# Kernel tuning notes

Hardware: AMD Instinct MI355X
Metric: run time of the kernel (lower is better)

The kernel has to match this reference:

```python
import jax, jax.numpy as jnp
import numpy as np

L, H, HS, D, T, V, B = 6, 6, 64, 384, 256, 65, 64
EPS = 1e-5


def layer_norm(x, g, b):
    m = x.mean(-1, keepdims=True)
    v = x.var(-1, keepdims=True)
    return (x - m) / jnp.sqrt(v + EPS) * g + b


def setup_inputs() -> dict:
    key = jax.random.key(0)
    ks = jax.random.split(key, 12)
    s = 0.02
    return {
        "idx": jax.random.randint(ks[0], (B, T), 0, V),
        "targets": jax.random.randint(ks[1], (B, T), 0, V),
        "tok_emb": s * jax.random.normal(ks[2], (V, D), jnp.float32),
        "pos_emb": s * jax.random.normal(ks[3], (T, D), jnp.float32),
        "Wq": s * jax.random.normal(ks[4], (L, H, D, HS), jnp.float32),
        "Wk": s * jax.random.normal(ks[5], (L, H, D, HS), jnp.float32),
        "Wv": s * jax.random.normal(ks[6], (L, H, D, HS), jnp.float32),
        "Wproj": s * jax.random.normal(ks[7], (L, D, D), jnp.float32),
        "bproj": jnp.zeros((L, D), jnp.float32),
        "W1": s * jax.random.normal(ks[8], (L, D, 4 * D), jnp.float32),
        "b1": jnp.zeros((L, 4 * D), jnp.float32),
        "W2": s * jax.random.normal(ks[9], (L, 4 * D, D), jnp.float32),
        "b2": jnp.zeros((L, D), jnp.float32),
        "ln1_g": jnp.ones((L, D), jnp.float32),
        "ln1_b": jnp.zeros((L, D), jnp.float32),
        "lnf_g": jnp.ones((D,), jnp.float32),
        "lnf_b": jnp.zeros((D,), jnp.float32),
        "Whead": s * jax.random.normal(ks[10], (D, V), jnp.float32),
        "bhead": jnp.zeros((V,), jnp.float32),
    }


def reference(idx, targets, tok_emb, pos_emb, Wq, Wk, Wv, Wproj, bproj,
              W1, b1, W2, b2, ln1_g, ln1_b, lnf_g, lnf_b, Whead, bhead):
    b, t = idx.shape
    x = tok_emb[idx] + pos_emb[:t]  # [B,T,D]
    mask = jnp.tril(jnp.ones((t, t), bool))
    scale = x.shape[-1] ** -0.5  # NOTE: original scales by n_emb_d**-0.5, not head_size**-0.5
    for l in range(L):
        y = layer_norm(x, ln1_g[l], ln1_b[l])
        q = jnp.einsum('btd,hde->bhte', y, Wq[l])
        k = jnp.einsum('btd,hde->bhte', y, Wk[l])
        v = jnp.einsum('btd,hde->bhte', y, Wv[l])
        w = jnp.einsum('bhte,bhse->bhts', q, k) * scale
        w = jnp.where(mask, w, -jnp.inf)
        w = jax.nn.softmax(w, axis=-1)
        o = jnp.einsum('bhts,bhse->bhte', w, v)
        o = o.transpose(0, 2, 1, 3).reshape(b, t, H * HS)  # concat heads on last dim
        x = x + o @ Wproj[l] + bproj[l]
        # NOTE: original Block reuses ln1 (not ln2) before the FFN -- replicated faithfully
        y2 = layer_norm(x, ln1_g[l], ln1_b[l])
        x = x + jax.nn.relu(y2 @ W1[l] + b1[l]) @ W2[l] + b2[l]
    x = layer_norm(x, lnf_g, lnf_b)
    logits = x @ Whead + bhead  # [B,T,V]
    logp = jax.nn.log_softmax(logits, axis=-1)
    loss = -jnp.take_along_axis(logp, targets[..., None], axis=-1).mean()
    return logits, loss
```

## Files before the change

kernel.cpp:

```cpp
#include <hip/hip_runtime.h>
#include <math.h>

#define L_ 6
#define H_ 6
#define HS_ 64
#define D_ 384
#define T_ 256
#define V_ 65
#define B_ 64
#define ROWS (B_*T_)
#define QKVN 1152
#define EPS_ 1e-5f

typedef __attribute__((ext_vector_type(8))) __bf16 bf16x8;
typedef __attribute__((ext_vector_type(4))) float f32x4;

__device__ __forceinline__ bf16x8 u4_to_bf8(uint4 u) {
    return __builtin_bit_cast(bf16x8, u);
}

__device__ __forceinline__ void glds16(const void* g, void* l) {
    __builtin_amdgcn_global_load_lds(
        (const __attribute__((address_space(1))) void*)g,
        (__attribute__((address_space(3))) void*)l, 16, 0, 0);
}

__global__ void embed_kernel(const int* __restrict__ idx,
                             const float* __restrict__ tok,
                             const float* __restrict__ pos,
                             float* __restrict__ x) {
    int i = blockIdx.x * blockDim.x + threadIdx.x;
    int d = i % D_;
    int row = i / D_;
    int t = row % T_;
    x[i] = tok[idx[row]*D_ + d] + pos[t*D_ + d];
}

__global__ __launch_bounds__(256)
void ln4(const float* __restrict__ x,
         const float* __restrict__ g,
         const float* __restrict__ b,
         __bf16* __restrict__ yb) {
    int w = threadIdx.x >> 6, lane = threadIdx.x & 63;
    int row = blockIdx.x * 4 + w;
    const float* xr = x + (size_t)row * D_;
    float v[6];
    #pragma unroll
    for (int i = 0; i < 6; ++i) v[i] = xr[lane + 64*i];
    float s = 0.f, sq = 0.f;
    #pragma unroll
    for (int i = 0; i < 6; ++i) { s += v[i]; sq += v[i]*v[i]; }
    for (int off = 32; off; off >>= 1) {
        s  += __shfl_xor(s,  off);
        sq += __shfl_xor(sq, off);
    }
    float mean = s * (1.0f/D_);
    float var  = sq * (1.0f/D_) - mean*mean;
    float rstd = rsqrtf(var + EPS_);
    __bf16* yr = yb + (size_t)row * D_;
    #pragma unroll
    for (int i = 0; i < 6; ++i) {
        int c = lane + 64*i;
        yr[c] = (__bf16)((v[i]-mean)*rstd*g[c] + b[c]);
    }
}

__global__ __launch_bounds__(256)
void transpose_cast(const float* __restrict__ src, __bf16* __restrict__ dst,
                    int R, int C, int zdiv, long sA, long sB, long dbase)
{
    __shared__ float tile[32][33];
    int z = blockIdx.z;
    const float* s = src + (long)z * R * C;
    __bf16* d = dst + dbase + (long)(z / zdiv) * sA + (long)(z % zdiv) * sB;
    int c0 = blockIdx.x * 32, r0 = blockIdx.y * 32;
    int t = threadIdx.x;
    int tr = t >> 3, tc = (t & 7) * 4;
    float4 v = *(const float4*)(s + (long)(r0 + tr) * C + c0 + tc);
    tile[tr][tc+0] = v.x; tile[tr][tc+1] = v.y;
    tile[tr][tc+2] = v.z; tile[tr][tc+3] = v.w;
    __syncthreads();
    #pragma unroll
    for (int j = 0; j < 4; ++j)
        d[(long)(c0 + tr) * R + r0 + tc + j] = (__bf16)tile[tc+j][tr];
}

__global__ __launch_bounds__(256)
void head_prep(const float* __restrict__ Whead, __bf16* __restrict__ headT) {
    int i = blockIdx.x * 256 + threadIdx.x;
    int n = i / D_, k = i % D_;
    headT[i] = (n < V_) ? (__bf16)Whead[k*V_ + n] : (__bf16)0.0f;
}

template<int TM>
__global__ __launch_bounds__(256)
void gemm_t(const __bf16* __restrict__ A, const __bf16* __restrict__ Bt,
            const float* __restrict__ bias, const float* res,
            float* outF, __bf16* outB,
            int K, int ldc, int ncols, int relu)
{
    constexpr int MI = TM / 32;
    __shared__ __align__(16) __bf16 As[2][TM*32];
    __shared__ __align__(16) __bf16 Bs[2][128*32];
    int t = threadIdx.x;
    int w = t >> 6, lane = t & 63;
    int ln = lane & 15, quad = lane >> 4;
    int n0 = blockIdx.x * 128, m0 = blockIdx.y * TM;
    int wm = (w >> 1) * (TM/2), wn = (w & 1) * 64;

    f32x4 acc[MI][4] = {};

    const char* Ab = (const char*)A + (size_t)m0 * K * 2;
    const char* Bb = (const char*)Bt + (size_t)n0 * K * 2;
    int f0 = w*64 + lane, f1 = f0 + 256;
    int r0 = f0 >> 2, r1 = f1 >> 2;
    size_t ga0 = (size_t)r0 * K * 2 + (size_t)(((f0 & 3) ^ (r0 & 3)) * 16);
    size_t ga1 = (size_t)r1 * K * 2 + (size_t)(((f1 & 3) ^ (r1 & 3)) * 16);
    int lo0 = w*64*16, lo1 = (w*64 + 256)*16;

    int nIt = K >> 5;
    glds16(Ab + ga0, (char*)As[0] + lo0);
    if constexpr (TM == 128) glds16(Ab + ga1, (char*)As[0] + lo1);
    glds16(Bb + ga0, (char*)Bs[0] + lo0);
    glds16(Bb + ga1, (char*)Bs[0] + lo1);

    for (int it = 0; it < nIt; ++it) {
        int p = it & 1;
        __syncthreads();
        if (it + 1 < nIt) {
            size_t kb = (size_t)(it + 1) * 64;
            glds16(Ab + ga0 + kb, (char*)As[p^1] + lo0);
            if constexpr (TM == 128) glds16(Ab + ga1 + kb, (char*)As[p^1] + lo1);
            glds16(Bb + ga0 + kb, (char*)Bs[p^1] + lo0);
            glds16(Bb + ga1 + kb, (char*)Bs[p^1] + lo1);
        }
        bf16x8 af[MI], bfr[4];
        #pragma unroll
        for (int i = 0; i < MI; ++i) {
            int row = wm + i*16 + ln;
            af[i] = __builtin_bit_cast(bf16x8,
                *(const uint4*)&As[p][row*32 + ((quad ^ (row & 3)) * 8)]);
        }
        #pragma unroll
        for (int j = 0; j < 4; ++j) {
            int row = wn + j*16 + ln;
            bfr[j] = __builtin_bit_cast(bf16x8,
                *(const uint4*)&Bs[p][row*32 + ((quad ^ (row & 3)) * 8)]);
        }
        #pragma unroll
        for (int i = 0; i < MI; ++i)
            #pragma unroll
            for (int j = 0; j < 4; ++j)
                acc[i][j] = __builtin_amdgcn_mfma_f32_16x16x32_bf16(
                                af[i], bfr[j], acc[i][j], 0, 0, 0);
        __syncthreads();
    }
    #pragma unroll
    for (int i = 0; i < MI; ++i) {
        #pragma unroll
        for (int r = 0; r < 4; ++r) {
            int row = m0 + wm + i*16 + quad*4 + r;
            #pragma unroll
            for (int j = 0; j < 4; ++j) {
                int col = n0 + wn + j*16 + ln;
                if (col < ncols) {
                    float v = acc[i][j][r];
                    if (bias) v += bias[col];
                    if (relu) v = fmaxf(v, 0.f);
                    if (res)  v += res[(size_t)row*ldc + col];
                    if (outF) outF[(size_t)row*ldc + col] = v;
                    if (outB) outB[(size_t)row*ldc + col] = (__bf16)v;
                }
            }
        }
    }
}

__global__ __launch_bounds__(256, 2)
void attn4(const __bf16* __restrict__ qkv, __bf16* __restrict__ o)
{
    __shared__ __align__(16) __bf16 Ks[256*72];
    __shared__ __align__(16) __bf16 Vt[64*264];
    __shared__ __align__(16) __bf16 Pw[4][32*40];
    int bid = blockIdx.x;
    int h = bid % H_;
    int b = bid / H_;
    int t = threadIdx.x;
    int w = t >> 6, lane = t & 63;
    int ln = lane & 15, quad = lane >> 4;
    const size_t rowb = (size_t)b * T_ * QKVN;
    const int hoff = h * HS_;
    const float scale = 0.05103103630798288f;

    for (int c = t; c < 2048; c += 256) {
        int r = c >> 3, e0 = (c & 7) * 8;
        uint4 uk = *(const uint4*)(qkv + rowb + (size_t)r*QKVN + 384 + hoff + e0);
        *(uint4*)&Ks[r*72 + e0] = uk;
        uint4 uv = *(const uint4*)(qkv + rowb + (size_t)r*QKVN + 768 + hoff + e0);
        bf16x8 v8 = u4_to_bf8(uv);
        #pragma unroll
        for (int j = 0; j < 8; ++j) {
            int e = e0 + j;
            Vt[e*264 + (((r >> 3) ^ ((e >> 3) & 3)) * 8) + (r & 7)] = v8[j];
        }
    }

    int qis[2] = { w, 7 - w };
    uint4 Qf[2][2][2];
    #pragma unroll
    for (int tl = 0; tl < 2; ++tl)
        #pragma unroll
        for (int mi = 0; mi < 2; ++mi)
            #pragma unroll
            for (int kc = 0; kc < 2; ++kc)
                Qf[tl][mi][kc] = *(const uint4*)(qkv + rowb +
                    (size_t)(qis[tl]*32 + mi*16 + ln)*QKVN + hoff + kc*32 + quad*8);

    __syncthreads();

    __bf16* P = Pw[w];
    #pragma unroll
    for (int tl = 0; tl < 2; ++tl) {
        int qi = qis[tl];
        f32x4 O[2][4] = {};
        float mst[2][4], lst[2][4];
        #pragma unroll
        for (int mi = 0; mi < 2; ++mi)
            #pragma unroll
            for (int r = 0; r < 4; ++r) { mst[mi][r] = -INFINITY; lst[mi][r] = 0.f; }

        for (int st = 0; st <= qi; ++st) {
            int sb = st * 32;
            f32x4 S[2][2] = {};
            #pragma unroll
            for (int kc = 0; kc < 2; ++kc) {
                uint4 Kf[2];
                #pragma unroll
                for (int ji = 0; ji < 2; ++ji)
                    Kf[ji] = *(const uint4*)&Ks[(sb + ji*16 + ln)*72 + kc*32 + quad*8];
                #pragma unroll
                for (int mi = 0; mi < 2; ++mi) {
                    bf16x8 qa = __builtin_bit_cast(bf16x8, Qf[tl][mi][kc]);
                    #pragma unroll
                    for (int ji = 0; ji < 2; ++ji)
                        S[mi][ji] = __builtin_amdgcn_mfma_f32_16x16x32_bf16(
                            qa, __builtin_bit_cast(bf16x8, Kf[ji]), S[mi][ji], 0, 0, 0);
                }
            }
            int diag = (st == qi);
            #pragma unroll
            for (int mi = 0; mi < 2; ++mi)
                #pragma unroll
                for (int ji = 0; ji < 2; ++ji)
                    #pragma unroll
                    for (int r = 0; r < 4; ++r) {
                        float v = S[mi][ji][r] * scale;
                        if (diag && (ji*16 + ln) > (mi*16 + quad*4 + r)) v = -INFINITY;
                        S[mi][ji][r] = v;
                    }
            #pragma unroll
            for (int mi = 0; mi < 2; ++mi)
                #pragma unroll
                for (int r = 0; r < 4; ++r) {
                    float mx = fmaxf(S[mi][0][r], S[mi][1][r]);
                    #pragma unroll
                    for (int off = 1; off < 16; off <<= 1)
                        mx = fmaxf(mx, __shfl_xor(mx, off));
                    float mn = fmaxf(mst[mi][r], mx);
                    float al = __expf(mst[mi][r] - mn);
                    mst[mi][r] = mn;
                    float p0 = __expf(S[mi][0][r] - mn);
                    float p1 = __expf(S[mi][1][r] - mn);
                    S[mi][0][r] = p0; S[mi][1][r] = p1;
                    float rs = p0 + p1;
                    #pragma unroll
                    for (int off = 1; off < 16; off <<= 1)
                        rs += __shfl_xor(rs, off);
                    lst[mi][r] = lst[mi][r]*al + rs;
                    #pragma unroll
                    for (int ei = 0; ei < 4; ++ei) O[mi][ei][r] *= al;
                }
            #pragma unroll
            for (int mi = 0; mi < 2; ++mi)
                #pragma unroll
                for (int ji = 0; ji < 2; ++ji)
                    #pragma unroll
                    for (int r = 0; r < 4; ++r)
                        P[(mi*16 + quad*4 + r)*40 + ji*16 + ln] = (__bf16)S[mi][ji][r];
            uint4 Pf[2], Vf[4];
            #pragma unroll
            for (int mi = 0; mi < 2; ++mi)
                Pf[mi] = *(const uint4*)&P[(mi*16 + ln)*40 + quad*8];
            #pragma unroll
            for (int ei = 0; ei < 4; ++ei) {
                int e = ei*16 + ln;
                Vf[ei] = *(const uint4*)&Vt[e*264 + (((st*4 + quad) ^ ((e >> 3) & 3)) * 8)];
            }
            #pragma unroll
            for (int mi = 0; mi < 2; ++mi)
                #pragma unroll
                for (int ei = 0; ei < 4; ++ei)
                    O[mi][ei] = __builtin_amdgcn_mfma_f32_16x16x32_bf16(
                        __builtin_bit_cast(bf16x8, Pf[mi]),
                        __builtin_bit_cast(bf16x8, Vf[ei]), O[mi][ei], 0, 0, 0);
        }
        #pragma unroll
        for (int mi = 0; mi < 2; ++mi)
            #pragma unroll
            for (int r = 0; r < 4; ++r) {
                float inv = 1.0f / lst[mi][r];
                size_t row = (size_t)(b*T_ + qi*32 + mi*16 + quad*4 + r);
                #pragma unroll
                for (int ei = 0; ei < 4; ++ei)
                    o[row*D_ + hoff + ei*16 + ln] = (__bf16)(O[mi][ei][r] * inv);
            }
    }
}

__global__ __launch_bounds__(256)
void loss2(const float* __restrict__ logits,
           const int* __restrict__ tg,
           float* __restrict__ loss)
{
    int row = blockIdx.x * 256 + threadIdx.x;
    const float* lr = logits + (size_t)row * V_;
    float m = -INFINITY;
    for (int c = 0; c < V_; ++c) m = fmaxf(m, lr[c]);
    float s = 0.f;
    for (int c = 0; c < V_; ++c) s += __expf(lr[c] - m);
    float val = -(lr[tg[row]] - m - __logf(s)) * (1.0f/ROWS);
    for (int off = 32; off; off >>= 1) val += __shfl_xor(val, off);
    __shared__ float red[4];
    int w = threadIdx.x >> 6, lane = threadIdx.x & 63;
    if (lane == 0) red[w] = val;
    __syncthreads();
    if (threadIdx.x == 0)
        atomicAdd(loss, red[0]+red[1]+red[2]+red[3]);
}

extern "C" void kernel_launch(void* const* d_in, const int* in_sizes, int n_in,
                              void* d_out, int out_size, void* d_ws, size_t ws_size,
                              hipStream_t stream)
{
    const int*   idx     = (const int*)  d_in[0];
    const int*   targets = (const int*)  d_in[1];
    const float* tok     = (const float*)d_in[2];
    const float* pos     = (const float*)d_in[3];
    const float* Wq      = (const float*)d_in[4];
    const float* Wk      = (const float*)d_in[5];
    const float* Wv      = (const float*)d_in[6];
    const float* Wproj   = (const float*)d_in[7];
    const float* bproj   = (const float*)d_in[8];
    const float* W1      = (const float*)d_in[9];
    const float* b1      = (const float*)d_in[10];
    const float* W2      = (const float*)d_in[11];
    const float* b2      = (const float*)d_in[12];
    const float* ln1g    = (const float*)d_in[13];
    const float* ln1b    = (const float*)d_in[14];
    const float* lnfg    = (const float*)d_in[15];
    const float* lnfb    = (const float*)d_in[16];
    const float* Whead   = (const float*)d_in[17];
    const float* bhead   = (const float*)d_in[18];

    float* logits = (float*)d_out;
    float* loss   = logits + (size_t)ROWS * V_;

    const size_t SZ = (size_t)ROWS * D_;
    const size_t RGELEMS = (size_t)ROWS * 4 * D_;

    float*  x   = (float*)d_ws;
    __bf16* yb  = (__bf16*)(x + SZ);
    __bf16* Rg  = yb + SZ;
    __bf16* qkv = Rg;
    __bf16* hid = Rg;
    __bf16* o   = Rg + RGELEMS;
    __bf16* qkvT  = o + SZ;
    __bf16* projT = qkvT + (size_t)L_*QKVN*D_;
    __bf16* w1T   = projT + (size_t)L_*D_*D_;
    __bf16* w2T   = w1T + (size_t)L_*D_*4*D_;
    __bf16* headT = w2T + (size_t)L_*D_*4*D_;

    transpose_cast<<<dim3(2,12,36),256,0,stream>>>(Wq, qkvT, D_, HS_, H_,
        (long)QKVN*D_, (long)HS_*D_, 0L);
    transpose_cast<<<dim3(2,12,36),256,0,stream>>>(Wk, qkvT, D_, HS_, H_,
        (long)QKVN*D_, (long)HS_*D_, (long)D_*D_);
    transpose_cast<<<dim3(2,12,36),256,0,stream>>>(Wv, qkvT, D_, HS_, H_,
        (long)QKVN*D_, (long)HS_*D_, 2L*D_*D_);
    transpose_cast<<<dim3(12,12,6),256,0,stream>>>(Wproj, projT, D_, D_, 1,
        (long)D_*D_, 0L, 0L);
    transpose_cast<<<dim3(48,12,6),256,0,stream>>>(W1, w1T, D_, 4*D_, 1,
        (long)D_*4*D_, 0L, 0L);
    transpose_cast<<<dim3(12,48,6),256,0,stream>>>(W2, w2T, 4*D_, D_, 1,
        (long)D_*4*D_, 0L, 0L);
    head_prep<<<(128*D_)/256, 256, 0, stream>>>(Whead, headT);

    embed_kernel<<<(ROWS*D_)/256, 256, 0, stream>>>(idx, tok, pos, x);

    for (int l = 0; l < L_; ++l) {
        ln4<<<ROWS/4, 256, 0, stream>>>(x, ln1g + l*D_, ln1b + l*D_, yb);
        gemm_t<128><<<dim3(QKVN/128, ROWS/128), 256, 0, stream>>>(
            yb, qkvT + (size_t)l*QKVN*D_, nullptr, nullptr, nullptr, qkv,
            D_, QKVN, QKVN, 0);
        attn4<<<B_*H_, 256, 0, stream>>>(qkv, o);
        gemm_t<64><<<dim3(D_/128, ROWS/64), 256, 0, stream>>>(
            o, projT + (size_t)l*D_*D_, bproj + l*D_, x, x, nullptr,
            D_, D_, D_, 0);
        ln4<<<ROWS/4, 256, 0, stream>>>(x, ln1g + l*D_, ln1b + l*D_, yb);
        gemm_t<128><<<dim3(4*D_/128, ROWS/128), 256, 0, stream>>>(
            yb, w1T + (size_t)l*D_*4*D_, b1 + l*4*D_, nullptr, nullptr, hid,
            D_, 4*D_, 4*D_, 1);
        gemm_t<64><<<dim3(D_/128, ROWS/64), 256, 0, stream>>>(
            hid, w2T + (size_t)l*D_*4*D_, b2 + l*D_, x, x, nullptr,
            4*D_, D_, D_, 0);
    }
    ln4<<<ROWS/4, 256, 0, stream>>>(x, lnfg, lnfb, yb);
    gemm_t<64><<<dim3(1, ROWS/64), 256, 0, stream>>>(
        yb, headT, bhead, nullptr, logits, nullptr,
        D_, V_, V_, 0);
    hipMemsetAsync(loss, 0, sizeof(float), stream);
    loss2<<<ROWS/256, 256, 0, stream>>>(logits, targets, loss);
}
```

Before: 1.529 ms.

## Add A-stationary GEMM keeping full K=384 row tile in LDS, streaming B from global

```diff
diff --git a/kernel.cpp b/kernel.cpp
--- a/kernel.cpp
+++ b/kernel.cpp
@@ -90,6 +90,80 @@
     int i = blockIdx.x * 256 + threadIdx.x;
     int n = i / D_, k = i % D_;
     headT[i] = (n < V_) ? (__bf16)Whead[k*V_ + n] : (__bf16)0.0f;
+}
+
+__global__ __launch_bounds__(256)
+void gemm_as(const __bf16* __restrict__ A, const __bf16* __restrict__ Bt,
+             const float* __restrict__ bias, const float* res,
+             float* outF, __bf16* outB,
+             int N, int ldc, int ncols, int relu)
+{
+    __shared__ __align__(16) __bf16 As[64*392];
+    int t = threadIdx.x;
+    int w = t >> 6, lane = t & 63;
+    int ln = lane & 15, quad = lane >> 4;
+    int m0 = blockIdx.x * 64;
+
+    for (int c = t; c < 3072; c += 256) {
+        int r = c / 48, ch = c - r*48;
+        uint4 v = *(const uint4*)(A + (size_t)(m0 + r)*384 + ch*8);
+        *(uint4*)&As[r*392 + ch*8] = v;
+    }
+    __syncthreads();
+
+    int nch = N >> 6;
+    for (int nc = w; nc < nch; nc += 4) {
+        int n0 = nc * 64;
+        const __bf16* Bp = Bt + (size_t)n0 * 384;
+        f32x4 acc[4][4] = {};
+        uint4 bcur[4], bnxt[4];
+        #pragma unroll
+        for (int j = 0; j < 4; ++j)
+            bcur[j] = *(const uint4*)(Bp + (size_t)(j*16 + ln)*384 + quad*8);
+        #pragma unroll
+        for (int kc = 0; kc < 12; ++kc) {
+            if (kc < 11) {
+                #pragma unroll
+                for (int j = 0; j < 4; ++j)
+                    bnxt[j] = *(const uint4*)(Bp + (size_t)(j*16 + ln)*384
+                                              + (kc+1)*32 + quad*8);
+            }
+            uint4 af[4];
+            #pragma unroll
+            for (int i = 0; i < 4; ++i)
+                af[i] = *(const uint4*)&As[(i*16 + ln)*392 + kc*32 + quad*8];
+            #pragma unroll
+            for (int i = 0; i < 4; ++i)
+                #pragma unroll
+                for (int j = 0; j < 4; ++j)
+                    acc[i][j] = __builtin_amdgcn_mfma_f32_16x16x32_bf16(
+                        __builtin_bit_cast(bf16x8, af[i]),
+                        __builtin_bit_cast(bf16x8, bcur[j]), acc[i][j], 0, 0, 0);
+            if (kc < 11) {
+                #pragma unroll
+                for (int j = 0; j < 4; ++j) bcur[j] = bnxt[j];
+            }
+        }
+        #pragma unroll
+        for (int i = 0; i < 4; ++i) {
+            #pragma unroll
+            for (int r = 0; r < 4; ++r) {
+                int row = m0 + i*16 + quad*4 + r;
+                #pragma unroll
+                for (int j = 0; j < 4; ++j) {
+                    int col = n0 + j*16 + ln;
+                    if (col < ncols) {
+                        float v = acc[i][j][r];
+                        if (bias) v += bias[col];
+                        if (relu) v = fmaxf(v, 0.f);
+                        if (res)  v += res[(size_t)row*ldc + col];
+                        if (outF) outF[(size_t)row*ldc + col] = v;
+                        if (outB) outB[(size_t)row*ldc + col] = (__bf16)v;
+                    }
+                }
+            }
+        }
+    }
 }
 
 template<int TM>
@@ -398,25 +472,25 @@
 
     for (int l = 0; l < L_; ++l) {
         ln4<<<ROWS/4, 256, 0, stream>>>(x, ln1g + l*D_, ln1b + l*D_, yb);
-        gemm_t<128><<<dim3(QKVN/128, ROWS/128), 256, 0, stream>>>(
+        gemm_as<<<ROWS/64, 256, 0, stream>>>(
             yb, qkvT + (size_t)l*QKVN*D_, nullptr, nullptr, nullptr, qkv,
-            D_, QKVN, QKVN, 0);
+            QKVN, QKVN, QKVN, 0);
         attn4<<<B_*H_, 256, 0, stream>>>(qkv, o);
-        gemm_t<64><<<dim3(D_/128, ROWS/64), 256, 0, stream>>>(
+        gemm_as<<<ROWS/64, 256, 0, stream>>>(
             o, projT + (size_t)l*D_*D_, bproj + l*D_, x, x, nullptr,
             D_, D_, D_, 0);
         ln4<<<ROWS/4, 256, 0, stream>>>(x, ln1g + l*D_, ln1b + l*D_, yb);
-        gemm_t<128><<<dim3(4*D_/128, ROWS/128), 256, 0, stream>>>(
+        gemm_as<<<ROWS/64, 256, 0, stream>>>(
             yb, w1T + (size_t)l*D_*4*D_, b1 + l*4*D_, nullptr, nullptr, hid,
-            D_, 4*D_, 4*D_, 1);
+            4*D_, 4*D_, 4*D_, 1);
         gemm_t<64><<<dim3(D_/128, ROWS/64), 256, 0, stream>>>(
             hid, w2T + (size_t)l*D_*4*D_, b2 + l*D_, x, x, nullptr,
             4*D_, D_, D_, 0);
     }
     ln4<<<ROWS/4, 256, 0, stream>>>(x, lnfg, lnfb, yb);
-    gemm_t<64><<<dim3(1, ROWS/64), 256, 0, stream>>>(
+    gemm_as<<<ROWS/64, 256, 0, stream>>>(
         yb, headT, bhead, nullptr, logits, nullptr,
-        D_, V_, V_, 0);
+        128, V_, V_, 0);
     hipMemsetAsync(loss, 0, sizeof(float), stream);
     loss2<<<ROWS/256, 256, 0, stream>>>(logits, targets, loss);
 }
```

New measurement: 2.233 ms. +46.0%, slower.
